# Optimization experiments

Hardware: AMD Instinct MI355X
Metric: run time of the kernel (lower is better)

Reference implementation:

```python
import jax, jax.numpy as jnp
import numpy as np

DIM = 192; HEADS = 6; HDIM = DIM // HEADS
WS = (2, 8, 8); SS = (1, 4, 4)
B, D, H, W = 2, 8, 64, 64
N = WS[0] * WS[1] * WS[2]          # 128 tokens per window
MLP_H = int(DIM * 2.0)
SCALE = HDIM ** -0.5


def _rel_pos_index_np():
    wd, wh, ww = WS
    coords = np.stack(np.meshgrid(np.arange(wd), np.arange(wh), np.arange(ww), indexing='ij'))
    cf = coords.reshape(3, -1)                      # (3, N)
    rel = (cf[:, :, None] - cf[:, None, :]).transpose(1, 2, 0)  # (N, N, 3)
    rel[..., 0] += wd - 1; rel[..., 1] += wh - 1; rel[..., 2] += ww - 1
    rel[..., 0] *= (2 * wh - 1) * (2 * ww - 1)
    rel[..., 1] *= (2 * ww - 1)
    return rel.sum(-1).astype(np.int32)            # (N, N)


def _compute_mask_np():
    wd, wh, ww = WS; sd, sh, sw = SS
    Dp = -(-D // wd) * wd; Hp = -(-H // wh) * wh; Wp = -(-W // ww) * ww
    img = np.zeros((1, Dp, Hp, Wp, 1), np.float32)
    cnt = 0
    for ds in (slice(0, -wd), slice(-wd, -sd), slice(-sd, None)):
        for hs in (slice(0, -wh), slice(-wh, -sh), slice(-sh, None)):
            for vs in (slice(0, -ww), slice(-ww, -sw), slice(-sw, None)):
                img[:, ds, hs, vs, :] = cnt; cnt += 1
    m = img.reshape(1, Dp // wd, wd, Hp // wh, wh, Wp // ww, ww, 1)
    m = m.transpose(0, 1, 3, 5, 2, 4, 6, 7).reshape(-1, N)       # (nW, N)
    am = m[:, None, :] - m[:, :, None]
    return np.where(am != 0, -100.0, 0.0).astype(np.float32)     # (nW, N, N)


def setup_inputs() -> dict:
    key = jax.random.key(0)
    ks = jax.random.split(key, 6)
    f = lambda k, s: (jax.random.normal(k, s, jnp.float32) * 0.02)
    n_bias = (2 * WS[0] - 1) * (2 * WS[1] - 1) * (2 * WS[2] - 1)  # 675
    return dict(
        x=jax.random.normal(ks[0], (B, D, H, W, DIM), jnp.float32),
        mask_matrix=jnp.asarray(_compute_mask_np()),
        rel_pos_index=jnp.asarray(_rel_pos_index_np()),
        gamma1=jnp.ones((DIM,), jnp.float32), beta1=jnp.zeros((DIM,), jnp.float32),
        w_qkv=f(ks[1], (3 * DIM, DIM)), b_qkv=jnp.zeros((3 * DIM,), jnp.float32),
        rpb=f(ks[2], (n_bias, HEADS)),
        w_proj=f(ks[3], (DIM, DIM)), b_proj=jnp.zeros((DIM,), jnp.float32),
        gamma2=jnp.ones((DIM,), jnp.float32), beta2=jnp.zeros((DIM,), jnp.float32),
        w_fc1=f(ks[4], (MLP_H, DIM)), b_fc1=jnp.zeros((MLP_H,), jnp.float32),
        w_fc2=f(ks[5], (DIM, MLP_H)), b_fc2=jnp.zeros((DIM,), jnp.float32),
    )


def _ln(x, g, b, eps=1e-5):
    mu = x.mean(-1, keepdims=True)
    var = ((x - mu) ** 2).mean(-1, keepdims=True)
    return (x - mu) * jax.lax.rsqrt(var + eps) * g + b


def _stl(x, mask, rpi, gamma1, beta1, w_qkv, b_qkv, rpb, w_proj, b_proj,
         gamma2, beta2, w_fc1, b_fc1, w_fc2, b_fc2):
    wd, wh, ww = WS; sd, sh, sw = SS
    # ---- part1: LN -> pad -> roll -> window attention -> reverse ----
    xn = _ln(x, gamma1, beta1)
    pd = (wd - D % wd) % wd; ph = (wh - H % wh) % wh; pw = (ww - W % ww) % ww
    xn = jnp.pad(xn, ((0, 0), (0, pd), (0, ph), (0, pw), (0, 0)))
    Dp, Hp, Wp = D + pd, H + ph, W + pw
    sx = jnp.roll(xn, (-sd, -sh, -sw), axis=(1, 2, 3))
    # window partition -> (Bw, N, C)
    xw = sx.reshape(B, Dp // wd, wd, Hp // wh, wh, Wp // ww, ww, DIM)
    xw = xw.transpose(0, 1, 3, 5, 2, 4, 6, 7).reshape(-1, N, DIM)
    Bw = xw.shape[0]
    qkv = (xw @ w_qkv.T + b_qkv).reshape(Bw, N, 3, HEADS, HDIM).transpose(2, 0, 3, 1, 4)
    q, k, v = qkv[0] * SCALE, qkv[1], qkv[2]
    attn = jnp.einsum('bhnd,bhmd->bhnm', q, k)
    bias = rpb[rpi.reshape(-1)].reshape(N, N, HEADS).transpose(2, 0, 1)  # (H, N, N)
    attn = attn + bias[None]
    nW = mask.shape[0]
    attn = (attn.reshape(Bw // nW, nW, HEADS, N, N) + mask[None, :, None]).reshape(Bw, HEADS, N, N)
    attn = jax.nn.softmax(attn, axis=-1)
    out = jnp.einsum('bhnm,bhmd->bhnd', attn, v).transpose(0, 2, 1, 3).reshape(Bw, N, DIM)
    out = out @ w_proj.T + b_proj
    # window reverse -> un-roll -> slice
    sx = out.reshape(B, Dp // wd, Hp // wh, Wp // ww, wd, wh, ww, DIM)
    sx = sx.transpose(0, 1, 4, 2, 5, 3, 6, 7).reshape(B, Dp, Hp, Wp, DIM)
    part1 = jnp.roll(sx, (sd, sh, sw), axis=(1, 2, 3))[:, :D, :H, :W, :]
    x = x + part1
    # ---- part2: LN -> MLP (GELU, exact) ----
    y = _ln(x, gamma2, beta2)
    h = jax.nn.gelu(y @ w_fc1.T + b_fc1, approximate=False)
    return x + (h @ w_fc2.T + b_fc2)


def reference(x, mask_matrix, rel_pos_index, gamma1, beta1, w_qkv, b_qkv, rpb,
              w_proj, b_proj, gamma2, beta2, w_fc1, b_fc1, w_fc2, b_fc2):
    return _stl(x, mask_matrix, rel_pos_index, gamma1, beta1, w_qkv, b_qkv, rpb,
                w_proj, b_proj, gamma2, beta2, w_fc1, b_fc1, w_fc2, b_fc2)
```

## Files before the change

### kernel.cpp

```cpp
#include <hip/hip_runtime.h>
#include <hip/hip_bf16.h>
#include <math.h>

#define TOKS   65536
#define DIMC   192
#define NTOK   128
#define MLPH   384
#define QSCALE 0.17677669529663687f

typedef unsigned short u16;
typedef unsigned int   u32;
typedef __attribute__((ext_vector_type(8))) short bf16x8;
typedef __attribute__((ext_vector_type(4))) float f32x4;

static __device__ __forceinline__ float gelu_exact(float v) {
    return 0.5f * v * (1.f + erff(v * 0.70710678118654752f));
}
static __device__ __forceinline__ u16 f2bf(float f) {
    __hip_bfloat16 h = __float2bfloat16(f);
    return *reinterpret_cast<u16*>(&h);
}
static __device__ __forceinline__ float bf2f(u16 b) {
    u32 u = ((u32)b) << 16;
    float f;
    __builtin_memcpy(&f, &u, 4);
    return f;
}
static __device__ __forceinline__ void gl_lds16(const u16* g, u16* l) {
    __builtin_amdgcn_global_load_lds(
        (const __attribute__((address_space(1))) void*)g,
        (__attribute__((address_space(3))) void*)l, 16, 0, 0);
}

#define OFF_XW   0u
#define OFF_Q    6291456u
#define OFF_K    12582912u
#define OFF_V    18874368u
#define OFF_BF   25165824u
#define OFF_WB   25264128u

__global__ __launch_bounds__(256) void k_cvt(const float* __restrict__ a,
                                             const float* __restrict__ b,
                                             const float* __restrict__ c,
                                             const float* __restrict__ d,
                                             u16* __restrict__ o) {
    int i = blockIdx.x * 256 + threadIdx.x;
    float v;
    if (i < 110592) v = a[i];
    else if (i < 147456) v = b[i - 110592];
    else if (i < 221184) v = c[i - 147456];
    else v = d[i - 221184];
    o[i] = f2bf(v);
}

__global__ __launch_bounds__(256) void k_bias(const float* __restrict__ rpb,
                                              const int* __restrict__ rpi,
                                              u16* __restrict__ biasw) {
    int idx = blockIdx.x * 256 + threadIdx.x;
    int h = idx >> 14;
    int n = (idx >> 7) & 127;
    int slot = idx & 127;
    int m = ((slot & 7) << 4) + (slot >> 3);
    biasw[idx] = f2bf(rpb[rpi[n * 128 + m] * 6 + h]);
}

template<bool PERMUTE>
__global__ __launch_bounds__(256) void k_ln(const float* __restrict__ x,
                                            const float* __restrict__ gamma,
                                            const float* __restrict__ beta,
                                            u16* __restrict__ out) {
    int tid  = threadIdx.x;
    int lane = tid & 63, wv = tid >> 6;
    int tk = blockIdx.x * 4 + wv;
    size_t src;
    if (PERMUTE) {
        int w_all = tk >> 7, t = tk & 127;
        int b  = w_all >> 8, rem = w_all & 255;
        int di = rem >> 6, hi = (rem >> 3) & 7, wi = rem & 7;
        int qd = (di * 2 + (t >> 6) + 1) & 7;
        int qh = (hi * 8 + ((t >> 3) & 7) + 4) & 63;
        int qw = (wi * 8 + (t & 7) + 4) & 63;
        src = ((size_t)(((b * 8 + qd) * 64 + qh) * 64 + qw)) * DIMC;
    } else {
        src = (size_t)tk * DIMC;
    }
    float v0 = x[src + lane];
    float v1 = x[src + 64 + lane];
    float v2 = x[src + 128 + lane];
    float s  = v0 + v1 + v2;
    float sq = v0 * v0 + v1 * v1 + v2 * v2;
    #pragma unroll
    for (int off = 32; off; off >>= 1) {
        s  += __shfl_xor(s, off);
        sq += __shfl_xor(sq, off);
    }
    float mu   = s * (1.f / 192.f);
    float var  = sq * (1.f / 192.f) - mu * mu;
    float rstd = rsqrtf(var + 1e-5f);
    size_t o = (size_t)tk * DIMC;
    out[o + lane]       = f2bf((v0 - mu) * rstd * gamma[lane]       + beta[lane]);
    out[o + 64 + lane]  = f2bf((v1 - mu) * rstd * gamma[64 + lane]  + beta[64 + lane]);
    out[o + 128 + lane] = f2bf((v2 - mu) * rstd * gamma[128 + lane] + beta[128 + lane]);
}

template<int MODE, int KD>
__global__ __launch_bounds__(256) void k_mgemm(const u16* __restrict__ A,
                                               const u16* __restrict__ W,
                                               const float* __restrict__ bias,
                                               void* __restrict__ outp,
                                               const float* __restrict__ aux,
                                               u16* __restrict__ q_o,
                                               u16* __restrict__ k_o,
                                               u16* __restrict__ v_o) {
    __shared__ u16 As[2][128 * 64];
    const int tid = threadIdx.x;
    const int wv = tid >> 6, l = tid & 63;
    const int l15 = l & 15, g4 = l >> 4;
    const int wm = wv >> 1, wn = wv & 1;
    const size_t m0 = (size_t)blockIdx.x * 128;
    const int n0 = blockIdx.y * 64;
    const int srow = l >> 3, scol = l & 7;

    f32x4 acc[4][2] = {};

    auto STAGE = [&](int b, int t) {
        const u16* Ab = A + m0 * KD + t * 64;
        #pragma unroll
        for (int j = 0; j < 4; ++j) {
            int row = (wv * 4 + j) * 8 + srow;
            int sc  = scol ^ (row & 7);
            gl_lds16(Ab + (size_t)row * KD + sc * 8, &As[b][(wv * 4 + j) * 512]);
        }
    };
    auto COMPUTE = [&](int b, int t) {
        #pragma unroll
        for (int kk = 0; kk < 2; ++kk) {
            bf16x8 bfr[2];
            #pragma unroll
            for (int nt = 0; nt < 2; ++nt)
                bfr[nt] = *(const bf16x8*)&W[(size_t)(n0 + wn * 32 + nt * 16 + l15) * KD
                                             + t * 64 + kk * 32 + g4 * 8];
            #pragma unroll
            for (int mt = 0; mt < 4; ++mt) {
                int row  = wm * 64 + mt * 16 + l15;
                int slot = (kk * 4 + g4) ^ (row & 7);
                bf16x8 afr = *(const bf16x8*)&As[b][row * 64 + slot * 8];
                #pragma unroll
                for (int nt = 0; nt < 2; ++nt)
                    acc[mt][nt] = __builtin_amdgcn_mfma_f32_16x16x32_bf16(afr, bfr[nt],
                                                                          acc[mt][nt], 0, 0, 0);
            }
        }
    };

    constexpr int NT = KD / 64;
    STAGE(0, 0);
    __syncthreads();
    for (int t = 0; t < NT; ++t) {
        if (t + 1 < NT) STAGE((t + 1) & 1, t + 1);
        COMPUTE(t & 1, t);
        __syncthreads();
    }

    #pragma unroll
    for (int mt = 0; mt < 4; ++mt) {
        #pragma unroll
        for (int nt = 0; nt < 2; ++nt) {
            int n  = n0 + wn * 32 + nt * 16 + l15;
            float bb = bias[n];
            int t0 = wm * 64 + mt * 16 + g4 * 4;
            if (MODE == 0) {
                int sel = (n >= 384) ? 2 : (n >= 192 ? 1 : 0);
                int rem = n - sel * 192;
                int head = rem >> 5, dd = rem & 31;
                int w = (int)(m0 >> 7);
                size_t b9 = (size_t)(w * 6 + head) * 4096;
                if (sel < 2) {
                    u16* dst = sel ? k_o : q_o;
                    float scl = sel ? 1.f : QSCALE;
                    #pragma unroll
                    for (int reg = 0; reg < 4; ++reg)
                        dst[b9 + (size_t)(t0 + reg) * 32 + dd] = f2bf((acc[mt][nt][reg] + bb) * scl);
                } else {
                    ushort4 uv;
                    uv.x = f2bf(acc[mt][nt][0] + bb); uv.y = f2bf(acc[mt][nt][1] + bb);
                    uv.z = f2bf(acc[mt][nt][2] + bb); uv.w = f2bf(acc[mt][nt][3] + bb);
                    *(ushort4*)&v_o[b9 + (size_t)dd * 128 + t0] = uv;
                }
            } else if (MODE == 1) {
                float* out = (float*)outp;
                #pragma unroll
                for (int reg = 0; reg < 4; ++reg) {
                    int m = (int)m0 + wm * 64 + mt * 16 + g4 * 4 + reg;
                    int w_all = m >> 7, tt = m & 127;
                    int b  = w_all >> 8, rem = w_all & 255;
                    int di = rem >> 6, hi = (rem >> 3) & 7, wi = rem & 7;
                    int qd = (di * 2 + (tt >> 6) + 1) & 7;
                    int qh = (hi * 8 + ((tt >> 3) & 7) + 4) & 63;
                    int qw = (wi * 8 + (tt & 7) + 4) & 63;
                    size_t dtok = (size_t)(((b * 8 + qd) * 64 + qh) * 64 + qw);
                    out[dtok * DIMC + n] = acc[mt][nt][reg] + bb + aux[dtok * DIMC + n];
                }
            } else if (MODE == 2) {
                u16* out = (u16*)outp;
                #pragma unroll
                for (int reg = 0; reg < 4; ++reg) {
                    size_t m = m0 + t0 + reg;
                    out[m * MLPH + n] = f2bf(gelu_exact(acc[mt][nt][reg] + bb));
                }
            } else {
                float* out = (float*)outp;
                #pragma unroll
                for (int reg = 0; reg < 4; ++reg) {
                    size_t m = m0 + t0 + reg;
                    out[m * DIMC + n] = acc[mt][nt][reg] + bb + aux[m * DIMC + n];
                }
            }
        }
    }
}

__global__ __launch_bounds__(256) void k_attn(const u16* __restrict__ qb,
                                              const u16* __restrict__ kb,
                                              const u16* __restrict__ vb,
                                              const u16* __restrict__ biasw,
                                              u16* __restrict__ attn_out) {
    __shared__ u16 Pl[4][32 * 128];
    int wh = blockIdx.x;
    int w_all = wh / 6, head = wh - w_all * 6;
    int wl = w_all & 255;
    int tid = threadIdx.x;
    int wv = tid >> 6, l = tid & 63;
    int l15 = l & 15, g4 = l >> 4;
    size_t base = (size_t)wh * 4096;
    const u16* qg = qb + base;
    const u16* kg = kb + base;
    const u16* vg = vb + base;
    int rowb = wv * 32;

    bf16x8 qa[2];
    #pragma unroll
    for (int rt = 0; rt < 2; ++rt)
        qa[rt] = *(const bf16x8*)&qg[(size_t)(rowb + rt * 16 + l15) * 32 + g4 * 8];

    f32x4 s[2][8] = {};
    #pragma unroll
    for (int ct = 0; ct < 8; ++ct) {
        bf16x8 kf = *(const bf16x8*)&kg[(size_t)(ct * 16 + l15) * 32 + g4 * 8];
        s[0][ct] = __builtin_amdgcn_mfma_f32_16x16x32_bf16(qa[0], kf, s[0][ct], 0, 0, 0);
        s[1][ct] = __builtin_amdgcn_mfma_f32_16x16x32_bf16(qa[1], kf, s[1][ct], 0, 0, 0);
    }

    int di = wl >> 6, hi = (wl >> 3) & 7, wi = wl & 7;
    auto rcode = [&](int t) {
        int d = di * 2 + (t >> 6);
        int h = hi * 8 + ((t >> 3) & 7);
        int w = wi * 8 + (t & 7);
        int rd = (d < 6) ? 0 : (d < 7 ? 1 : 2);
        int rh = (h < 56) ? 0 : (h < 60 ? 1 : 2);
        int rw = (w < 56) ? 0 : (w < 60 ? 1 : 2);
        return rd * 9 + rh * 3 + rw;
    };
    int rm[8];
    #pragma unroll
    for (int ct = 0; ct < 8; ++ct) rm[ct] = rcode(ct * 16 + l15);

    const u16* bh = biasw + (size_t)head * 16384;
    #pragma unroll
    for (int rt = 0; rt < 2; ++rt)
        #pragma unroll
        for (int reg = 0; reg < 4; ++reg) {
            int n = rowb + rt * 16 + g4 * 4 + reg;
            int rn = rcode(n);
            bf16x8 bv = *(const bf16x8*)&bh[(size_t)n * 128 + l15 * 8];
            #pragma unroll
            for (int ct = 0; ct < 8; ++ct) {
                float mval = (rn == rm[ct]) ? 0.f : -100.f;
                s[rt][ct][reg] += bf2f((u16)bv[ct]) + mval;
            }
        }

    u16* Pw = Pl[wv];
    #pragma unroll
    for (int rt = 0; rt < 2; ++rt)
        #pragma unroll
        for (int reg = 0; reg < 4; ++reg) {
            float mx = -1e30f;
            #pragma unroll
            for (int ct = 0; ct < 8; ++ct) mx = fmaxf(mx, s[rt][ct][reg]);
            #pragma unroll
            for (int off = 1; off < 16; off <<= 1) mx = fmaxf(mx, __shfl_xor(mx, off));
            float sum = 0.f;
            #pragma unroll
            for (int ct = 0; ct < 8; ++ct) {
                float p = __expf(s[rt][ct][reg] - mx);
                s[rt][ct][reg] = p; sum += p;
            }
            #pragma unroll
            for (int off = 1; off < 16; off <<= 1) sum += __shfl_xor(sum, off);
            float inv = 1.f / sum;
            int nloc = rt * 16 + g4 * 4 + reg;
            int sw = ((nloc >> 2) & 3) << 4;
            #pragma unroll
            for (int ct = 0; ct < 8; ++ct) {
                int m = ct * 16 + l15;
                Pw[nloc * 128 + (m ^ sw)] = f2bf(s[rt][ct][reg] * inv);
            }
        }
    __syncthreads();

    f32x4 o[2][2] = {};
    #pragma unroll
    for (int kt = 0; kt < 4; ++kt) {
        bf16x8 vf[2];
        #pragma unroll
        for (int dt = 0; dt < 2; ++dt)
            vf[dt] = *(const bf16x8*)&vg[(size_t)(dt * 16 + l15) * 128 + kt * 32 + g4 * 8];
        #pragma unroll
        for (int rt = 0; rt < 2; ++rt) {
            int nloc = rt * 16 + l15;
            int sw = ((nloc >> 2) & 3) << 4;
            int m8 = kt * 32 + g4 * 8;
            bf16x8 pa = *(const bf16x8*)&Pw[nloc * 128 + (m8 ^ sw)];
            #pragma unroll
            for (int dt = 0; dt < 2; ++dt)
                o[rt][dt] = __builtin_amdgcn_mfma_f32_16x16x32_bf16(pa, vf[dt], o[rt][dt], 0, 0, 0);
        }
    }

    #pragma unroll
    for (int rt = 0; rt < 2; ++rt)
        #pragma unroll
        for (int dt = 0; dt < 2; ++dt)
            #pragma unroll
            for (int reg = 0; reg < 4; ++reg) {
                int n = rowb + rt * 16 + g4 * 4 + reg;
                int d = dt * 16 + l15;
                attn_out[((size_t)(w_all * 128 + n)) * DIMC + head * 32 + d] = f2bf(o[rt][dt][reg]);
            }
}

extern "C" void kernel_launch(void* const* d_in, const int* in_sizes, int n_in,
                              void* d_out, int out_size, void* d_ws, size_t ws_size,
                              hipStream_t stream) {
    const float* x      = (const float*)d_in[0];
    const int*   rpi    = (const int*)d_in[2];
    const float* gamma1 = (const float*)d_in[3];
    const float* beta1  = (const float*)d_in[4];
    const float* w_qkv  = (const float*)d_in[5];
    const float* b_qkv  = (const float*)d_in[6];
    const float* rpb    = (const float*)d_in[7];
    const float* w_proj = (const float*)d_in[8];
    const float* b_proj = (const float*)d_in[9];
    const float* gamma2 = (const float*)d_in[10];
    const float* beta2  = (const float*)d_in[11];
    const float* w_fc1  = (const float*)d_in[12];
    const float* b_fc1  = (const float*)d_in[13];
    const float* w_fc2  = (const float*)d_in[14];
    const float* b_fc2  = (const float*)d_in[15];

    float* ws    = (float*)d_ws;
    u16*   xwu   = (u16*)(ws + OFF_XW);
    u16*   qbu   = (u16*)(ws + OFF_Q);
    u16*   kbu   = (u16*)(ws + OFF_K);
    u16*   vbu   = (u16*)(ws + OFF_V);
    u16*   hbu   = (u16*)(ws + OFF_Q);
    u16*   ybu   = (u16*)(ws + OFF_V);
    u16*   biasw = (u16*)(ws + OFF_BF);
    u16*   wb    = (u16*)(ws + OFF_WB);
    float* xres  = (float*)d_out;

    const u16* wqkv_b = wb;
    const u16* wproj_b = wb + 110592;
    const u16* wfc1_b = wb + 147456;
    const u16* wfc2_b = wb + 221184;

    k_cvt<<<1152, 256, 0, stream>>>(w_qkv, w_proj, w_fc1, w_fc2, wb);
    k_bias<<<384, 256, 0, stream>>>(rpb, rpi, biasw);
    k_ln<true><<<16384, 256, 0, stream>>>(x, gamma1, beta1, xwu);
    k_mgemm<0, 192><<<dim3(512, 9), 256, 0, stream>>>(xwu, wqkv_b, b_qkv, nullptr, nullptr,
                                                      qbu, kbu, vbu);
    k_attn<<<3072, 256, 0, stream>>>(qbu, kbu, vbu, biasw, xwu);
    k_mgemm<1, 192><<<dim3(512, 3), 256, 0, stream>>>(xwu, wproj_b, b_proj, xres, x,
                                                      nullptr, nullptr, nullptr);
    k_ln<false><<<16384, 256, 0, stream>>>(xres, gamma2, beta2, ybu);
    k_mgemm<2, 192><<<dim3(512, 6), 256, 0, stream>>>(ybu, wfc1_b, b_fc1, hbu, nullptr,
                                                      nullptr, nullptr, nullptr);
    k_mgemm<3, 384><<<dim3(512, 3), 256, 0, stream>>>(hbu, wfc2_b, b_fc2, xres, xres,
                                                      nullptr, nullptr, nullptr);
}
```

Baseline: 222.2 us.

## Fuse LayerNorm into GEMM prologues and loop all N tiles per block

The separate LayerNorm kernels are removed. LN1 (with the window permute) and LN2 are now computed directly into the GEMM's shared-memory A tile. Each GEMM block now keeps its full 128x192 (or half of the 384) A panel resident in LDS and loops over every N tile, instead of launching a 2D grid that reloads A for each N tile. This removes two launches and the bf16 round trips of the normalized activations, and cuts repeated A loads. In exchange the grid is only 512 blocks with serial N loops, the old double-buffered staging that overlapped loads with compute is gone, and the LDS footprint grows, which may limit occupancy and latency hiding.

Result: no change. 225.3 us (+1.4%).

```diff
diff --git a/kernel.cpp b/kernel.cpp
--- a/kernel.cpp
+++ b/kernel.cpp
@@ -64,159 +64,172 @@
     biasw[idx] = f2bf(rpb[rpi[n * 128 + m] * 6 + h]);
 }
 
-template<bool PERMUTE>
-__global__ __launch_bounds__(256) void k_ln(const float* __restrict__ x,
-                                            const float* __restrict__ gamma,
-                                            const float* __restrict__ beta,
-                                            u16* __restrict__ out) {
-    int tid  = threadIdx.x;
-    int lane = tid & 63, wv = tid >> 6;
-    int tk = blockIdx.x * 4 + wv;
-    size_t src;
-    if (PERMUTE) {
-        int w_all = tk >> 7, t = tk & 127;
-        int b  = w_all >> 8, rem = w_all & 255;
-        int di = rem >> 6, hi = (rem >> 3) & 7, wi = rem & 7;
-        int qd = (di * 2 + (t >> 6) + 1) & 7;
-        int qh = (hi * 8 + ((t >> 3) & 7) + 4) & 63;
-        int qw = (wi * 8 + (t & 7) + 4) & 63;
-        src = ((size_t)(((b * 8 + qd) * 64 + qh) * 64 + qw)) * DIMC;
-    } else {
-        src = (size_t)tk * DIMC;
-    }
-    float v0 = x[src + lane];
-    float v1 = x[src + 64 + lane];
-    float v2 = x[src + 128 + lane];
-    float s  = v0 + v1 + v2;
-    float sq = v0 * v0 + v1 * v1 + v2 * v2;
-    #pragma unroll
-    for (int off = 32; off; off >>= 1) {
-        s  += __shfl_xor(s, off);
-        sq += __shfl_xor(sq, off);
-    }
-    float mu   = s * (1.f / 192.f);
-    float var  = sq * (1.f / 192.f) - mu * mu;
-    float rstd = rsqrtf(var + 1e-5f);
-    size_t o = (size_t)tk * DIMC;
-    out[o + lane]       = f2bf((v0 - mu) * rstd * gamma[lane]       + beta[lane]);
-    out[o + 64 + lane]  = f2bf((v1 - mu) * rstd * gamma[64 + lane]  + beta[64 + lane]);
-    out[o + 128 + lane] = f2bf((v2 - mu) * rstd * gamma[128 + lane] + beta[128 + lane]);
-}
-
-template<int MODE, int KD>
-__global__ __launch_bounds__(256) void k_mgemm(const u16* __restrict__ A,
-                                               const u16* __restrict__ W,
-                                               const float* __restrict__ bias,
-                                               void* __restrict__ outp,
-                                               const float* __restrict__ aux,
-                                               u16* __restrict__ q_o,
-                                               u16* __restrict__ k_o,
-                                               u16* __restrict__ v_o) {
-    __shared__ u16 As[2][128 * 64];
+template<int MODE>
+__global__ __launch_bounds__(256) void k_fgemm(
+    const void* __restrict__ srcA, const u16* __restrict__ W,
+    const float* __restrict__ bias, void* __restrict__ outp,
+    const float* __restrict__ aux,
+    u16* __restrict__ q_o, u16* __restrict__ k_o, u16* __restrict__ v_o,
+    const float* __restrict__ gam, const float* __restrict__ bet)
+{
+    constexpr int KD = (MODE == 3) ? 384 : 192;
+    constexpr int NT = (MODE == 0) ? 9 : (MODE == 2 ? 6 : 3);
+    __shared__ u16 As[3 * 128 * 64];
     const int tid = threadIdx.x;
     const int wv = tid >> 6, l = tid & 63;
     const int l15 = l & 15, g4 = l >> 4;
     const int wm = wv >> 1, wn = wv & 1;
     const size_t m0 = (size_t)blockIdx.x * 128;
-    const int n0 = blockIdx.y * 64;
-    const int srow = l >> 3, scol = l & 7;
-
-    f32x4 acc[4][2] = {};
-
-    auto STAGE = [&](int b, int t) {
-        const u16* Ab = A + m0 * KD + t * 64;
-        #pragma unroll
-        for (int j = 0; j < 4; ++j) {
-            int row = (wv * 4 + j) * 8 + srow;
-            int sc  = scol ^ (row & 7);
-            gl_lds16(Ab + (size_t)row * KD + sc * 8, &As[b][(wv * 4 + j) * 512]);
+
+    auto STAGEP = [&](int p) {
+        const u16* Ab = (const u16*)srcA + m0 * KD + p * 192;
+        #pragma unroll
+        for (int j = 0; j < 12; ++j) {
+            int cid = j * 256 + wv * 64 + l;
+            int tile = cid >> 10, r = (cid >> 3) & 127, sl = cid & 7;
+            int sc = sl ^ (r & 7);
+            gl_lds16(Ab + (size_t)r * KD + tile * 64 + sc * 8,
+                     &As[(size_t)(j * 256 + wv * 64) * 8]);
         }
     };
-    auto COMPUTE = [&](int b, int t) {
-        #pragma unroll
-        for (int kk = 0; kk < 2; ++kk) {
-            bf16x8 bfr[2];
+
+    if (MODE == 0 || MODE == 2) {
+        const float* xs = (const float*)srcA;
+        float g0 = gam[l], g1 = gam[64 + l], g2 = gam[128 + l];
+        float b0 = bet[l], b1 = bet[64 + l], b2 = bet[128 + l];
+        for (int it = 0; it < 32; ++it) {
+            int t = it * 4 + wv;
+            size_t srcrow;
+            if (MODE == 0) {
+                int w_all = (int)blockIdx.x;
+                int b = w_all >> 8, rem = w_all & 255;
+                int di = rem >> 6, hi = (rem >> 3) & 7, wi = rem & 7;
+                int qd = (di * 2 + (t >> 6) + 1) & 7;
+                int qh = (hi * 8 + ((t >> 3) & 7) + 4) & 63;
+                int qw = (wi * 8 + (t & 7) + 4) & 63;
+                srcrow = ((size_t)(((b * 8 + qd) * 64 + qh) * 64 + qw)) * DIMC;
+            } else {
+                srcrow = (m0 + t) * DIMC;
+            }
+            float v0 = xs[srcrow + l], v1 = xs[srcrow + 64 + l], v2 = xs[srcrow + 128 + l];
+            float s = v0 + v1 + v2, sq = v0 * v0 + v1 * v1 + v2 * v2;
+            #pragma unroll
+            for (int off = 32; off; off >>= 1) { s += __shfl_xor(s, off); sq += __shfl_xor(sq, off); }
+            float mu = s * (1.f / 192.f);
+            float rstd = rsqrtf(sq * (1.f / 192.f) - mu * mu + 1e-5f);
+            int se = (((l >> 3) ^ (t & 7)) << 3) + (l & 7);
+            As[(0 * 128 + t) * 64 + se] = f2bf((v0 - mu) * rstd * g0 + b0);
+            As[(1 * 128 + t) * 64 + se] = f2bf((v1 - mu) * rstd * g1 + b1);
+            As[(2 * 128 + t) * 64 + se] = f2bf((v2 - mu) * rstd * g2 + b2);
+        }
+    } else {
+        STAGEP(0);
+    }
+    __syncthreads();
+
+    auto KSTEP = [&](f32x4 (&acc)[4][2], int n0, int kglob, int ktloc) {
+        bf16x8 bfr[2];
+        #pragma unroll
+        for (int nt = 0; nt < 2; ++nt)
+            bfr[nt] = *(const bf16x8*)&W[(size_t)(n0 + wn * 32 + nt * 16 + l15) * KD
+                                         + kglob * 32 + g4 * 8];
+        #pragma unroll
+        for (int mt = 0; mt < 4; ++mt) {
+            int row  = wm * 64 + mt * 16 + l15;
+            int slot = ((ktloc & 1) * 4 + g4) ^ (row & 7);
+            bf16x8 afr = *(const bf16x8*)&As[(size_t)((ktloc >> 1) * 128 + row) * 64 + slot * 8];
             #pragma unroll
             for (int nt = 0; nt < 2; ++nt)
-                bfr[nt] = *(const bf16x8*)&W[(size_t)(n0 + wn * 32 + nt * 16 + l15) * KD
-                                             + t * 64 + kk * 32 + g4 * 8];
-            #pragma unroll
-            for (int mt = 0; mt < 4; ++mt) {
-                int row  = wm * 64 + mt * 16 + l15;
-                int slot = (kk * 4 + g4) ^ (row & 7);
-                bf16x8 afr = *(const bf16x8*)&As[b][row * 64 + slot * 8];
-                #pragma unroll
-                for (int nt = 0; nt < 2; ++nt)
-                    acc[mt][nt] = __builtin_amdgcn_mfma_f32_16x16x32_bf16(afr, bfr[nt],
-                                                                          acc[mt][nt], 0, 0, 0);
-            }
+                acc[mt][nt] = __builtin_amdgcn_mfma_f32_16x16x32_bf16(afr, bfr[nt],
+                                                                      acc[mt][nt], 0, 0, 0);
         }
     };
 
-    constexpr int NT = KD / 64;
-    STAGE(0, 0);
-    __syncthreads();
-    for (int t = 0; t < NT; ++t) {
-        if (t + 1 < NT) STAGE((t + 1) & 1, t + 1);
-        COMPUTE(t & 1, t);
+    auto EPI = [&](int n0, f32x4 (&acc)[4][2]) {
+        #pragma unroll
+        for (int mt = 0; mt < 4; ++mt) {
+            #pragma unroll
+            for (int nt = 0; nt < 2; ++nt) {
+                int n  = n0 + wn * 32 + nt * 16 + l15;
+                float bb = bias[n];
+                int t0 = wm * 64 + mt * 16 + g4 * 4;
+                if (MODE == 0) {
+                    int sel = (n >= 384) ? 2 : (n >= 192 ? 1 : 0);
+                    int rem = n - sel * 192;
+                    int head = rem >> 5, dd = rem & 31;
+                    int w = (int)blockIdx.x;
+                    size_t b9 = (size_t)(w * 6 + head) * 4096;
+                    if (sel < 2) {
+                        u16* dst = sel ? k_o : q_o;
+                        float scl = sel ? 1.f : QSCALE;
+                        #pragma unroll
+                        for (int reg = 0; reg < 4; ++reg)
+                            dst[b9 + (size_t)(t0 + reg) * 32 + dd] = f2bf((acc[mt][nt][reg] + bb) * scl);
+                    } else {
+                        ushort4 uv;
+                        uv.x = f2bf(acc[mt][nt][0] + bb); uv.y = f2bf(acc[mt][nt][1] + bb);
+                        uv.z = f2bf(acc[mt][nt][2] + bb); uv.w = f2bf(acc[mt][nt][3] + bb);
+                        *(ushort4*)&v_o[b9 + (size_t)dd * 128 + t0] = uv;
+                    }
+                } else if (MODE == 1) {
+                    float* out = (float*)outp;
+                    #pragma unroll
+                    for (int reg = 0; reg < 4; ++reg) {
+                        int m = (int)m0 + t0 + reg;
+                        int w_all = m >> 7, tt = m & 127;
+                        int b  = w_all >> 8, rem = w_all & 255;
+                        int di = rem >> 6, hi = (rem >> 3) & 7, wi = rem & 7;
+                        int qd = (di * 2 + (tt >> 6) + 1) & 7;
+                        int qh = (hi * 8 + ((tt >> 3) & 7) + 4) & 63;
+                        int qw = (wi * 8 + (tt & 7) + 4) & 63;
+                        size_t dtok = (size_t)(((b * 8 + qd) * 64 + qh) * 64 + qw);
+                        out[dtok * DIMC + n] = acc[mt][nt][reg] + bb + aux[dtok * DIMC + n];
+                    }
+                } else if (MODE == 2) {
+                    u16* out = (u16*)outp;
+                    #pragma unroll
+                    for (int reg = 0; reg < 4; ++reg) {
+                        size_t m = m0 + t0 + reg;
+                        out[m * MLPH + n] = f2bf(gelu_exact(acc[mt][nt][reg] + bb));
+                    }
+                } else {
+                    float* out = (float*)outp;
+                    #pragma unroll
+                    for (int reg = 0; reg < 4; ++reg) {
+                        size_t m = m0 + t0 + reg;
+                        out[m * DIMC + n] = acc[mt][nt][reg] + bb + aux[m * DIMC + n];
+                    }
+                }
+            }
+        }
+    };
+
+    if (MODE != 3) {
+        #pragma unroll 1
+        for (int n0i = 0; n0i < NT; ++n0i) {
+            f32x4 acc[4][2] = {};
+            #pragma unroll
+            for (int kt = 0; kt < 6; ++kt) KSTEP(acc, n0i * 64, kt, kt);
+            EPI(n0i * 64, acc);
+        }
+    } else {
+        f32x4 a0[4][2] = {}, a1[4][2] = {}, a2[4][2] = {};
+        #pragma unroll 1
+        for (int kt = 0; kt < 6; ++kt) {
+            KSTEP(a0, 0,   kt, kt);
+            KSTEP(a1, 64,  kt, kt);
+            KSTEP(a2, 128, kt, kt);
+        }
         __syncthreads();
-    }
-
-    #pragma unroll
-    for (int mt = 0; mt < 4; ++mt) {
-        #pragma unroll
-        for (int nt = 0; nt < 2; ++nt) {
-            int n  = n0 + wn * 32 + nt * 16 + l15;
-            float bb = bias[n];
-            int t0 = wm * 64 + mt * 16 + g4 * 4;
-            if (MODE == 0) {
-                int sel = (n >= 384) ? 2 : (n >= 192 ? 1 : 0);
-                int rem = n - sel * 192;
-                int head = rem >> 5, dd = rem & 31;
-                int w = (int)(m0 >> 7);
-                size_t b9 = (size_t)(w * 6 + head) * 4096;
-                if (sel < 2) {
-                    u16* dst = sel ? k_o : q_o;
-                    float scl = sel ? 1.f : QSCALE;
-                    #pragma unroll
-                    for (int reg = 0; reg < 4; ++reg)
-                        dst[b9 + (size_t)(t0 + reg) * 32 + dd] = f2bf((acc[mt][nt][reg] + bb) * scl);
-                } else {
-                    ushort4 uv;
-                    uv.x = f2bf(acc[mt][nt][0] + bb); uv.y = f2bf(acc[mt][nt][1] + bb);
-                    uv.z = f2bf(acc[mt][nt][2] + bb); uv.w = f2bf(acc[mt][nt][3] + bb);
-                    *(ushort4*)&v_o[b9 + (size_t)dd * 128 + t0] = uv;
-                }
-            } else if (MODE == 1) {
-                float* out = (float*)outp;
-                #pragma unroll
-                for (int reg = 0; reg < 4; ++reg) {
-                    int m = (int)m0 + wm * 64 + mt * 16 + g4 * 4 + reg;
-                    int w_all = m >> 7, tt = m & 127;
-                    int b  = w_all >> 8, rem = w_all & 255;
-                    int di = rem >> 6, hi = (rem >> 3) & 7, wi = rem & 7;
-                    int qd = (di * 2 + (tt >> 6) + 1) & 7;
-                    int qh = (hi * 8 + ((tt >> 3) & 7) + 4) & 63;
-                    int qw = (wi * 8 + (tt & 7) + 4) & 63;
-                    size_t dtok = (size_t)(((b * 8 + qd) * 64 + qh) * 64 + qw);
-                    out[dtok * DIMC + n] = acc[mt][nt][reg] + bb + aux[dtok * DIMC + n];
-                }
-            } else if (MODE == 2) {
-                u16* out = (u16*)outp;
-                #pragma unroll
-                for (int reg = 0; reg < 4; ++reg) {
-                    size_t m = m0 + t0 + reg;
-                    out[m * MLPH + n] = f2bf(gelu_exact(acc[mt][nt][reg] + bb));
-                }
-            } else {
-                float* out = (float*)outp;
-                #pragma unroll
-                for (int reg = 0; reg < 4; ++reg) {
-                    size_t m = m0 + t0 + reg;
-                    out[m * DIMC + n] = acc[mt][nt][reg] + bb + aux[m * DIMC + n];
-                }
-            }
-        }
+        STAGEP(1);
+        __syncthreads();
+        #pragma unroll 1
+        for (int kt = 0; kt < 6; ++kt) {
+            KSTEP(a0, 0,   6 + kt, kt);
+            KSTEP(a1, 64,  6 + kt, kt);
+            KSTEP(a2, 128, 6 + kt, kt);
+        }
+        EPI(0, a0); EPI(64, a1); EPI(128, a2);
     }
 }
 
@@ -365,27 +378,24 @@
     u16*   kbu   = (u16*)(ws + OFF_K);
     u16*   vbu   = (u16*)(ws + OFF_V);
     u16*   hbu   = (u16*)(ws + OFF_Q);
-    u16*   ybu   = (u16*)(ws + OFF_V);
     u16*   biasw = (u16*)(ws + OFF_BF);
     u16*   wb    = (u16*)(ws + OFF_WB);
     float* xres  = (float*)d_out;
 
-    const u16* wqkv_b = wb;
+    const u16* wqkv_b  = wb;
     const u16* wproj_b = wb + 110592;
-    const u16* wfc1_b = wb + 147456;
-    const u16* wfc2_b = wb + 221184;
+    const u16* wfc1_b  = wb + 147456;
+    const u16* wfc2_b  = wb + 221184;
 
     k_cvt<<<1152, 256, 0, stream>>>(w_qkv, w_proj, w_fc1, w_fc2, wb);
     k_bias<<<384, 256, 0, stream>>>(rpb, rpi, biasw);
-    k_ln<true><<<16384, 256, 0, stream>>>(x, gamma1, beta1, xwu);
-    k_mgemm<0, 192><<<dim3(512, 9), 256, 0, stream>>>(xwu, wqkv_b, b_qkv, nullptr, nullptr,
-                                                      qbu, kbu, vbu);
+    k_fgemm<0><<<512, 256, 0, stream>>>(x, wqkv_b, b_qkv, nullptr, nullptr,
+                                        qbu, kbu, vbu, gamma1, beta1);
     k_attn<<<3072, 256, 0, stream>>>(qbu, kbu, vbu, biasw, xwu);
-    k_mgemm<1, 192><<<dim3(512, 3), 256, 0, stream>>>(xwu, wproj_b, b_proj, xres, x,
-                                                      nullptr, nullptr, nullptr);
-    k_ln<false><<<16384, 256, 0, stream>>>(xres, gamma2, beta2, ybu);
-    k_mgemm<2, 192><<<dim3(512, 6), 256, 0, stream>>>(ybu, wfc1_b, b_fc1, hbu, nullptr,
-                                                      nullptr, nullptr, nullptr);
-    k_mgemm<3, 384><<<dim3(512, 3), 256, 0, stream>>>(hbu, wfc2_b, b_fc2, xres, xres,
-                                                      nullptr, nullptr, nullptr);
-}
+    k_fgemm<1><<<512, 256, 0, stream>>>(xwu, wproj_b, b_proj, xres, x,
+                                        nullptr, nullptr, nullptr, nullptr, nullptr);
+    k_fgemm<2><<<512, 256, 0, stream>>>(xres, wfc1_b, b_fc1, hbu, nullptr,
+                                        nullptr, nullptr, nullptr, gamma2, beta2);
+    k_fgemm<3><<<512, 256, 0, stream>>>(hbu, wfc2_b, b_fc2, xres, xres,
+                                        nullptr, nullptr, nullptr, nullptr, nullptr);
+}
```

## Restructure GEMMs to keep weight tile in LDS and stream A into registers

Applied to the files above, without the earlier changes.

Replaces the A-in-LDS double-buffered GEMM with a kernel that loads the block's full 64-column weight slice into LDS once. Each block then processes several 128-row M tiles, reading A fragments straight from global memory into registers, with the next tile's loads issued while the current tile computes. This amortizes weight staging across 2-4 M tiles and removes the per-K-step barrier. The cost is fewer blocks, which lowers parallelism, plus heavy register use for the A fragments, which may lower occupancy.

Result: slower. 237.2 us (+6.8%).

```diff
diff --git a/kernel.cpp b/kernel.cpp
--- a/kernel.cpp
+++ b/kernel.cpp
@@ -30,6 +30,10 @@
     __builtin_amdgcn_global_load_lds(
         (const __attribute__((address_space(1))) void*)g,
         (__attribute__((address_space(3))) void*)l, 16, 0, 0);
+}
+static __device__ __forceinline__ f32x4 fz4() {
+    f32x4 z = {0.f, 0.f, 0.f, 0.f};
+    return z;
 }
 
 #define OFF_XW   0u
@@ -103,120 +107,159 @@
     out[o + 128 + lane] = f2bf((v2 - mu) * rstd * gamma[128 + lane] + beta[128 + lane]);
 }
 
-template<int MODE, int KD>
-__global__ __launch_bounds__(256) void k_mgemm(const u16* __restrict__ A,
-                                               const u16* __restrict__ W,
-                                               const float* __restrict__ bias,
-                                               void* __restrict__ outp,
-                                               const float* __restrict__ aux,
-                                               u16* __restrict__ q_o,
-                                               u16* __restrict__ k_o,
-                                               u16* __restrict__ v_o) {
-    __shared__ u16 As[2][128 * 64];
+template<int MODE>
+__global__ __launch_bounds__(256) void k_wgemm(
+    const u16* __restrict__ A, const u16* __restrict__ W,
+    const float* __restrict__ bias, void* __restrict__ outp,
+    const float* __restrict__ aux,
+    u16* __restrict__ q_o, u16* __restrict__ k_o, u16* __restrict__ v_o)
+{
+    constexpr int KD = (MODE == 3) ? 384 : 192;
+    constexpr int KT = KD / 64;
+    constexpr int NS = (MODE == 1 || MODE == 3) ? 2 : 4;
+    __shared__ u16 Ws[KT * 64 * 64];
     const int tid = threadIdx.x;
     const int wv = tid >> 6, l = tid & 63;
     const int l15 = l & 15, g4 = l >> 4;
-    const int wm = wv >> 1, wn = wv & 1;
-    const size_t m0 = (size_t)blockIdx.x * 128;
     const int n0 = blockIdx.y * 64;
-    const int srow = l >> 3, scol = l & 7;
-
-    f32x4 acc[4][2] = {};
-
-    auto STAGE = [&](int b, int t) {
-        const u16* Ab = A + m0 * KD + t * 64;
-        #pragma unroll
-        for (int j = 0; j < 4; ++j) {
-            int row = (wv * 4 + j) * 8 + srow;
-            int sc  = scol ^ (row & 7);
-            gl_lds16(Ab + (size_t)row * KD + sc * 8, &As[b][(wv * 4 + j) * 512]);
-        }
+
+    {
+        const u16* Wb = W + (size_t)n0 * KD;
+        #pragma unroll
+        for (int j = 0; j < KT * 2; ++j) {
+            int cid = j * 256 + tid;
+            int tile = cid >> 9, r = (cid >> 3) & 63, sl = cid & 7;
+            int sc = sl ^ (r & 7);
+            gl_lds16(Wb + (size_t)r * KD + tile * 64 + sc * 8,
+                     &Ws[(size_t)(j * 256 + wv * 64) * 8]);
+        }
+    }
+
+    f32x4 acc[2][4];
+    #pragma unroll
+    for (int mt = 0; mt < 2; ++mt)
+        #pragma unroll
+        for (int nt = 0; nt < 4; ++nt) acc[mt][nt] = fz4();
+
+    bf16x8 afA[2][6], afB[2][6];
+
+    auto LOADA = [&](bf16x8 (&af)[2][6], size_t m0, int kh) {
+        const u16* Ab = A + (m0 + (size_t)(wv * 32 + l15)) * KD + kh * 192;
+        #pragma unroll
+        for (int mt = 0; mt < 2; ++mt)
+            #pragma unroll
+            for (int kg = 0; kg < 6; ++kg)
+                af[mt][kg] = *(const bf16x8*)&Ab[(size_t)mt * 16 * KD + kg * 32 + g4 * 8];
     };
-    auto COMPUTE = [&](int b, int t) {
-        #pragma unroll
-        for (int kk = 0; kk < 2; ++kk) {
-            bf16x8 bfr[2];
-            #pragma unroll
-            for (int nt = 0; nt < 2; ++nt)
-                bfr[nt] = *(const bf16x8*)&W[(size_t)(n0 + wn * 32 + nt * 16 + l15) * KD
-                                             + t * 64 + kk * 32 + g4 * 8];
-            #pragma unroll
-            for (int mt = 0; mt < 4; ++mt) {
-                int row  = wm * 64 + mt * 16 + l15;
-                int slot = (kk * 4 + g4) ^ (row & 7);
-                bf16x8 afr = *(const bf16x8*)&As[b][row * 64 + slot * 8];
-                #pragma unroll
-                for (int nt = 0; nt < 2; ++nt)
-                    acc[mt][nt] = __builtin_amdgcn_mfma_f32_16x16x32_bf16(afr, bfr[nt],
-                                                                          acc[mt][nt], 0, 0, 0);
+    auto COMP = [&](bf16x8 (&af)[2][6], int kbase) {
+        #pragma unroll
+        for (int kg = 0; kg < 6; ++kg) {
+            int kgg = kbase + kg;
+            #pragma unroll
+            for (int nt = 0; nt < 4; ++nt) {
+                int r = nt * 16 + l15;
+                int slot = ((kgg & 1) * 4 + g4) ^ (r & 7);
+                bf16x8 wf = *(const bf16x8*)&Ws[(kgg >> 1) * 4096 + r * 64 + slot * 8];
+                acc[0][nt] = __builtin_amdgcn_mfma_f32_16x16x32_bf16(af[0][kg], wf, acc[0][nt], 0, 0, 0);
+                acc[1][nt] = __builtin_amdgcn_mfma_f32_16x16x32_bf16(af[1][kg], wf, acc[1][nt], 0, 0, 0);
             }
         }
     };
-
-    constexpr int NT = KD / 64;
-    STAGE(0, 0);
-    __syncthreads();
-    for (int t = 0; t < NT; ++t) {
-        if (t + 1 < NT) STAGE((t + 1) & 1, t + 1);
-        COMPUTE(t & 1, t);
+    auto ZERO = [&]() {
+        #pragma unroll
+        for (int mt = 0; mt < 2; ++mt)
+            #pragma unroll
+            for (int nt = 0; nt < 4; ++nt) acc[mt][nt] = fz4();
+    };
+    auto EPI = [&](size_t m0) {
+        int w = (int)(m0 >> 7);
+        #pragma unroll
+        for (int mt = 0; mt < 2; ++mt) {
+            int t0 = wv * 32 + mt * 16 + g4 * 4;
+            #pragma unroll
+            for (int nt = 0; nt < 4; ++nt) {
+                int n = n0 + nt * 16 + l15;
+                float bb = bias[n];
+                if (MODE == 0) {
+                    int sel = (n0 >= 384) ? 2 : (n0 >= 192 ? 1 : 0);
+                    int rem = n - sel * 192;
+                    int head = rem >> 5, dd = rem & 31;
+                    size_t b9 = (size_t)(w * 6 + head) * 4096;
+                    if (sel < 2) {
+                        u16* dst = sel ? k_o : q_o;
+                        float scl = sel ? 1.f : QSCALE;
+                        #pragma unroll
+                        for (int reg = 0; reg < 4; ++reg)
+                            dst[b9 + (size_t)(t0 + reg) * 32 + dd] =
+                                f2bf((acc[mt][nt][reg] + bb) * scl);
+                    } else {
+                        ushort4 uv;
+                        uv.x = f2bf(acc[mt][nt][0] + bb); uv.y = f2bf(acc[mt][nt][1] + bb);
+                        uv.z = f2bf(acc[mt][nt][2] + bb); uv.w = f2bf(acc[mt][nt][3] + bb);
+                        *(ushort4*)&v_o[b9 + (size_t)dd * 128 + t0] = uv;
+                    }
+                } else if (MODE == 1) {
+                    float* out = (float*)outp;
+                    #pragma unroll
+                    for (int reg = 0; reg < 4; ++reg) {
+                        int m = (int)m0 + t0 + reg;
+                        int w_all = m >> 7, tt = m & 127;
+                        int b  = w_all >> 8, rem = w_all & 255;
+                        int di = rem >> 6, hi = (rem >> 3) & 7, wi = rem & 7;
+                        int qd = (di * 2 + (tt >> 6) + 1) & 7;
+                        int qh = (hi * 8 + ((tt >> 3) & 7) + 4) & 63;
+                        int qw = (wi * 8 + (tt & 7) + 4) & 63;
+                        size_t dtok = (size_t)(((b * 8 + qd) * 64 + qh) * 64 + qw);
+                        out[dtok * DIMC + n] = acc[mt][nt][reg] + bb + aux[dtok * DIMC + n];
+                    }
+                } else if (MODE == 2) {
+                    u16* out = (u16*)outp;
+                    #pragma unroll
+                    for (int reg = 0; reg < 4; ++reg) {
+                        size_t m = m0 + t0 + reg;
+                        out[m * MLPH + n] = f2bf(gelu_exact(acc[mt][nt][reg] + bb));
+                    }
+                } else {
+                    float* out = (float*)outp;
+                    #pragma unroll
+                    for (int reg = 0; reg < 4; ++reg) {
+                        size_t m = m0 + t0 + reg;
+                        out[m * DIMC + n] = acc[mt][nt][reg] + bb + aux[m * DIMC + n];
+                    }
+                }
+            }
+        }
+    };
+
+    const size_t s0 = (size_t)blockIdx.x * NS * 128;
+    if (MODE == 3) {
+        LOADA(afA, s0, 0);
+        LOADA(afB, s0, 1);
         __syncthreads();
-    }
-
-    #pragma unroll
-    for (int mt = 0; mt < 4; ++mt) {
-        #pragma unroll
-        for (int nt = 0; nt < 2; ++nt) {
-            int n  = n0 + wn * 32 + nt * 16 + l15;
-            float bb = bias[n];
-            int t0 = wm * 64 + mt * 16 + g4 * 4;
-            if (MODE == 0) {
-                int sel = (n >= 384) ? 2 : (n >= 192 ? 1 : 0);
-                int rem = n - sel * 192;
-                int head = rem >> 5, dd = rem & 31;
-                int w = (int)(m0 >> 7);
-                size_t b9 = (size_t)(w * 6 + head) * 4096;
-                if (sel < 2) {
-                    u16* dst = sel ? k_o : q_o;
-                    float scl = sel ? 1.f : QSCALE;
-                    #pragma unroll
-                    for (int reg = 0; reg < 4; ++reg)
-                        dst[b9 + (size_t)(t0 + reg) * 32 + dd] = f2bf((acc[mt][nt][reg] + bb) * scl);
-                } else {
-                    ushort4 uv;
-                    uv.x = f2bf(acc[mt][nt][0] + bb); uv.y = f2bf(acc[mt][nt][1] + bb);
-                    uv.z = f2bf(acc[mt][nt][2] + bb); uv.w = f2bf(acc[mt][nt][3] + bb);
-                    *(ushort4*)&v_o[b9 + (size_t)dd * 128 + t0] = uv;
-                }
-            } else if (MODE == 1) {
-                float* out = (float*)outp;
-                #pragma unroll
-                for (int reg = 0; reg < 4; ++reg) {
-                    int m = (int)m0 + wm * 64 + mt * 16 + g4 * 4 + reg;
-                    int w_all = m >> 7, tt = m & 127;
-                    int b  = w_all >> 8, rem = w_all & 255;
-                    int di = rem >> 6, hi = (rem >> 3) & 7, wi = rem & 7;
-                    int qd = (di * 2 + (tt >> 6) + 1) & 7;
-                    int qh = (hi * 8 + ((tt >> 3) & 7) + 4) & 63;
-                    int qw = (wi * 8 + (tt & 7) + 4) & 63;
-                    size_t dtok = (size_t)(((b * 8 + qd) * 64 + qh) * 64 + qw);
-                    out[dtok * DIMC + n] = acc[mt][nt][reg] + bb + aux[dtok * DIMC + n];
-                }
-            } else if (MODE == 2) {
-                u16* out = (u16*)outp;
-                #pragma unroll
-                for (int reg = 0; reg < 4; ++reg) {
-                    size_t m = m0 + t0 + reg;
-                    out[m * MLPH + n] = f2bf(gelu_exact(acc[mt][nt][reg] + bb));
-                }
-            } else {
-                float* out = (float*)outp;
-                #pragma unroll
-                for (int reg = 0; reg < 4; ++reg) {
-                    size_t m = m0 + t0 + reg;
-                    out[m * DIMC + n] = acc[mt][nt][reg] + bb + aux[m * DIMC + n];
-                }
-            }
-        }
+        COMP(afA, 0);
+        LOADA(afA, s0 + 128, 0);
+        COMP(afB, 6);
+        EPI(s0); ZERO();
+        LOADA(afB, s0 + 128, 1);
+        COMP(afA, 0);
+        COMP(afB, 6);
+        EPI(s0 + 128);
+    } else if (MODE == 1) {
+        LOADA(afA, s0, 0);
+        LOADA(afB, s0 + 128, 0);
+        __syncthreads();
+        COMP(afA, 0); EPI(s0); ZERO();
+        COMP(afB, 0); EPI(s0 + 128);
+    } else {
+        LOADA(afA, s0, 0);
+        LOADA(afB, s0 + 128, 0);
+        __syncthreads();
+        COMP(afA, 0); EPI(s0); ZERO();
+        LOADA(afA, s0 + 256, 0);
+        COMP(afB, 0); EPI(s0 + 128); ZERO();
+        LOADA(afB, s0 + 384, 0);
+        COMP(afA, 0); EPI(s0 + 256); ZERO();
+        COMP(afB, 0); EPI(s0 + 384);
     }
 }
 
@@ -370,22 +413,22 @@
     u16*   wb    = (u16*)(ws + OFF_WB);
     float* xres  = (float*)d_out;
 
-    const u16* wqkv_b = wb;
+    const u16* wqkv_b  = wb;
     const u16* wproj_b = wb + 110592;
-    const u16* wfc1_b = wb + 147456;
-    const u16* wfc2_b = wb + 221184;
+    const u16* wfc1_b  = wb + 147456;
+    const u16* wfc2_b  = wb + 221184;
 
     k_cvt<<<1152, 256, 0, stream>>>(w_qkv, w_proj, w_fc1, w_fc2, wb);
     k_bias<<<384, 256, 0, stream>>>(rpb, rpi, biasw);
     k_ln<true><<<16384, 256, 0, stream>>>(x, gamma1, beta1, xwu);
-    k_mgemm<0, 192><<<dim3(512, 9), 256, 0, stream>>>(xwu, wqkv_b, b_qkv, nullptr, nullptr,
-                                                      qbu, kbu, vbu);
+    k_wgemm<0><<<dim3(128, 9), 256, 0, stream>>>(xwu, wqkv_b, b_qkv, nullptr, nullptr,
+                                                 qbu, kbu, vbu);
     k_attn<<<3072, 256, 0, stream>>>(qbu, kbu, vbu, biasw, xwu);
-    k_mgemm<1, 192><<<dim3(512, 3), 256, 0, stream>>>(xwu, wproj_b, b_proj, xres, x,
-                                                      nullptr, nullptr, nullptr);
+    k_wgemm<1><<<dim3(256, 3), 256, 0, stream>>>(xwu, wproj_b, b_proj, xres, x,
+                                                 nullptr, nullptr, nullptr);
     k_ln<false><<<16384, 256, 0, stream>>>(xres, gamma2, beta2, ybu);
-    k_mgemm<2, 192><<<dim3(512, 6), 256, 0, stream>>>(ybu, wfc1_b, b_fc1, hbu, nullptr,
-                                                      nullptr, nullptr, nullptr);
-    k_mgemm<3, 384><<<dim3(512, 3), 256, 0, stream>>>(hbu, wfc2_b, b_fc2, xres, xres,
-                                                      nullptr, nullptr, nullptr);
-}
+    k_wgemm<2><<<dim3(128, 6), 256, 0, stream>>>(ybu, wfc1_b, b_fc1, hbu, nullptr,
+                                                 nullptr, nullptr, nullptr);
+    k_wgemm<3><<<dim3(256, 3), 256, 0, stream>>>(hbu, wfc2_b, b_fc2, xres, xres,
+                                                 nullptr, nullptr, nullptr);
+}
```

## Stage GEMM and attention epilogues through LDS for vectorized coalesced stores

Applied to the files above, without the earlier changes.

The GEMM epilogues now write their accumulators into the freed shared-memory tile with an XOR swizzle, then read back whole rows and issue 16-byte vectorized global stores. This covers the q/k/v scatter, the GELU output, and the fp32 residual adds, which also load aux as float4. The attention kernel's output likewise goes through LDS so each thread stores 8 bf16 at once instead of scattered 2-byte writes. The goal is to remove uncoalesced narrow global writes, at the cost of extra barriers and LDS round trips in the epilogue.

Measured after the change: 216.7 us. 1.03x faster.

```diff
diff --git a/kernel.cpp b/kernel.cpp
--- a/kernel.cpp
+++ b/kernel.cpp
@@ -113,6 +113,8 @@
                                                u16* __restrict__ k_o,
                                                u16* __restrict__ v_o) {
     __shared__ u16 As[2][128 * 64];
+    u16*   Eu = (u16*)As;
+    float* Ef = (float*)As;
     const int tid = threadIdx.x;
     const int wv = tid >> 6, l = tid & 63;
     const int l15 = l & 15, g4 = l >> 4;
@@ -162,60 +164,109 @@
         __syncthreads();
     }
 
-    #pragma unroll
-    for (int mt = 0; mt < 4; ++mt) {
-        #pragma unroll
-        for (int nt = 0; nt < 2; ++nt) {
-            int n  = n0 + wn * 32 + nt * 16 + l15;
-            float bb = bias[n];
-            int t0 = wm * 64 + mt * 16 + g4 * 4;
-            if (MODE == 0) {
-                int sel = (n >= 384) ? 2 : (n >= 192 ? 1 : 0);
-                int rem = n - sel * 192;
-                int head = rem >> 5, dd = rem & 31;
-                int w = (int)(m0 >> 7);
-                size_t b9 = (size_t)(w * 6 + head) * 4096;
-                if (sel < 2) {
-                    u16* dst = sel ? k_o : q_o;
-                    float scl = sel ? 1.f : QSCALE;
-                    #pragma unroll
-                    for (int reg = 0; reg < 4; ++reg)
-                        dst[b9 + (size_t)(t0 + reg) * 32 + dd] = f2bf((acc[mt][nt][reg] + bb) * scl);
-                } else {
-                    ushort4 uv;
-                    uv.x = f2bf(acc[mt][nt][0] + bb); uv.y = f2bf(acc[mt][nt][1] + bb);
-                    uv.z = f2bf(acc[mt][nt][2] + bb); uv.w = f2bf(acc[mt][nt][3] + bb);
-                    *(ushort4*)&v_o[b9 + (size_t)dd * 128 + t0] = uv;
-                }
-            } else if (MODE == 1) {
-                float* out = (float*)outp;
+    const int w = (int)(m0 >> 7);
+
+    if (MODE == 0 || MODE == 2) {
+        const int sel = (MODE == 0) ? ((n0 >= 384) ? 2 : (n0 >= 192 ? 1 : 0)) : 0;
+        const float scl = (MODE == 0 && sel == 0) ? QSCALE : 1.f;
+        #pragma unroll
+        for (int mt = 0; mt < 4; ++mt) {
+            #pragma unroll
+            for (int nt = 0; nt < 2; ++nt) {
+                int c = wn * 32 + nt * 16 + l15;
+                float bb = bias[n0 + c];
                 #pragma unroll
                 for (int reg = 0; reg < 4; ++reg) {
-                    int m = (int)m0 + wm * 64 + mt * 16 + g4 * 4 + reg;
-                    int w_all = m >> 7, tt = m & 127;
-                    int b  = w_all >> 8, rem = w_all & 255;
-                    int di = rem >> 6, hi = (rem >> 3) & 7, wi = rem & 7;
-                    int qd = (di * 2 + (tt >> 6) + 1) & 7;
-                    int qh = (hi * 8 + ((tt >> 3) & 7) + 4) & 63;
-                    int qw = (wi * 8 + (tt & 7) + 4) & 63;
-                    size_t dtok = (size_t)(((b * 8 + qd) * 64 + qh) * 64 + qw);
-                    out[dtok * DIMC + n] = acc[mt][nt][reg] + bb + aux[dtok * DIMC + n];
+                    int r = wm * 64 + mt * 16 + g4 * 4 + reg;
+                    float v = acc[mt][nt][reg] + bb;
+                    if (MODE == 2) v = gelu_exact(v);
+                    else v *= scl;
+                    int slot8 = (c >> 3) ^ ((r >> 2) & 7);
+                    Eu[r * 64 + slot8 * 8 + (c & 7)] = f2bf(v);
                 }
-            } else if (MODE == 2) {
-                u16* out = (u16*)outp;
+            }
+        }
+        __syncthreads();
+        if (MODE == 2) {
+            u16* out = (u16*)outp;
+            #pragma unroll
+            for (int p = 0; p < 4; ++p) {
+                int cid = p * 256 + tid;
+                int r = cid >> 3, j = cid & 7;
+                int slot8 = j ^ ((r >> 2) & 7);
+                bf16x8 vv = *(const bf16x8*)&Eu[r * 64 + slot8 * 8];
+                *(bf16x8*)&out[(m0 + r) * MLPH + n0 + j * 8] = vv;
+            }
+        } else if (sel < 2) {
+            u16* dst = sel ? k_o : q_o;
+            const int hbase = (n0 - sel * 192) >> 5;
+            #pragma unroll
+            for (int p = 0; p < 4; ++p) {
+                int cid = p * 256 + tid;
+                int r = cid >> 3, j = cid & 7;
+                int c0 = j * 8;
+                int slot8 = j ^ ((r >> 2) & 7);
+                bf16x8 vv = *(const bf16x8*)&Eu[r * 64 + slot8 * 8];
+                size_t b9 = (size_t)(w * 6 + hbase + (c0 >> 5)) * 4096;
+                *(bf16x8*)&dst[b9 + (size_t)r * 32 + (c0 & 31)] = vv;
+            }
+        } else {
+            const int hbase = (n0 - 384) >> 5;
+            #pragma unroll
+            for (int p = 0; p < 4; ++p) {
+                int cid = p * 256 + tid;
+                int c = cid >> 4, jt = cid & 15;
+                int t0 = jt * 8;
+                u16 tmp[8];
+                #pragma unroll
+                for (int i = 0; i < 8; ++i) {
+                    int r = t0 + i;
+                    int slot8 = (c >> 3) ^ ((r >> 2) & 7);
+                    tmp[i] = Eu[r * 64 + slot8 * 8 + (c & 7)];
+                }
+                size_t b9 = (size_t)(w * 6 + hbase + (c >> 5)) * 4096;
+                *(bf16x8*)&v_o[b9 + (size_t)(c & 31) * 128 + t0] = *(bf16x8*)tmp;
+            }
+        }
+    } else {
+        #pragma unroll
+        for (int mt = 0; mt < 4; ++mt) {
+            #pragma unroll
+            for (int nt = 0; nt < 2; ++nt) {
+                int c = wn * 32 + nt * 16 + l15;
+                float bb = bias[n0 + c];
                 #pragma unroll
                 for (int reg = 0; reg < 4; ++reg) {
-                    size_t m = m0 + t0 + reg;
-                    out[m * MLPH + n] = f2bf(gelu_exact(acc[mt][nt][reg] + bb));
+                    int r = wm * 64 + mt * 16 + g4 * 4 + reg;
+                    int swz = (c >> 2) ^ ((r >> 2) & 3);
+                    Ef[r * 64 + swz * 4 + (c & 3)] = acc[mt][nt][reg] + bb;
                 }
+            }
+        }
+        __syncthreads();
+        float* out = (float*)outp;
+        #pragma unroll
+        for (int p = 0; p < 8; ++p) {
+            int cid = p * 256 + tid;
+            int r = cid >> 4, j = cid & 15;
+            int swz = j ^ ((r >> 2) & 3);
+            float4 vv = *(const float4*)&Ef[r * 64 + swz * 4];
+            size_t drow;
+            if (MODE == 1) {
+                int m = (int)m0 + r;
+                int w_all = m >> 7, tt = m & 127;
+                int b  = w_all >> 8, rem = w_all & 255;
+                int di = rem >> 6, hi = (rem >> 3) & 7, wi = rem & 7;
+                int qd = (di * 2 + (tt >> 6) + 1) & 7;
+                int qh = (hi * 8 + ((tt >> 3) & 7) + 4) & 63;
+                int qw = (wi * 8 + (tt & 7) + 4) & 63;
+                drow = (size_t)(((b * 8 + qd) * 64 + qh) * 64 + qw) * DIMC;
             } else {
-                float* out = (float*)outp;
-                #pragma unroll
-                for (int reg = 0; reg < 4; ++reg) {
-                    size_t m = m0 + t0 + reg;
-                    out[m * DIMC + n] = acc[mt][nt][reg] + bb + aux[m * DIMC + n];
-                }
-            }
+                drow = (m0 + r) * DIMC;
+            }
+            float4 ax = *(const float4*)&aux[drow + n0 + j * 4];
+            vv.x += ax.x; vv.y += ax.y; vv.z += ax.z; vv.w += ax.w;
+            *(float4*)&out[drow + n0 + j * 4] = vv;
         }
     }
 }
@@ -226,6 +277,7 @@
                                               const u16* __restrict__ biasw,
                                               u16* __restrict__ attn_out) {
     __shared__ u16 Pl[4][32 * 128];
+    u16* Ou = (u16*)Pl;
     int wh = blockIdx.x;
     int w_all = wh / 6, head = wh - w_all * 6;
     int wl = w_all & 255;
@@ -328,16 +380,27 @@
         }
     }
 
+    __syncthreads();
     #pragma unroll
     for (int rt = 0; rt < 2; ++rt)
         #pragma unroll
         for (int dt = 0; dt < 2; ++dt)
             #pragma unroll
             for (int reg = 0; reg < 4; ++reg) {
-                int n = rowb + rt * 16 + g4 * 4 + reg;
-                int d = dt * 16 + l15;
-                attn_out[((size_t)(w_all * 128 + n)) * DIMC + head * 32 + d] = f2bf(o[rt][dt][reg]);
-            }
+                int r = rowb + rt * 16 + g4 * 4 + reg;
+                int c = dt * 16 + l15;
+                int slot8 = (c >> 3) ^ ((r >> 2) & 3);
+                Ou[r * 32 + slot8 * 8 + (c & 7)] = f2bf(o[rt][dt][reg]);
+            }
+    __syncthreads();
+    #pragma unroll
+    for (int p = 0; p < 2; ++p) {
+        int cid = p * 256 + tid;
+        int r = cid >> 2, j = cid & 3;
+        int slot8 = j ^ ((r >> 2) & 3);
+        bf16x8 vv = *(const bf16x8*)&Ou[r * 32 + slot8 * 8];
+        *(bf16x8*)&attn_out[((size_t)(w_all * 128 + r)) * DIMC + head * 32 + j * 8] = vv;
+    }
 }
 
 extern "C" void kernel_launch(void* const* d_in, const int* in_sizes, int n_in,
@@ -370,10 +433,10 @@
     u16*   wb    = (u16*)(ws + OFF_WB);
     float* xres  = (float*)d_out;
 
-    const u16* wqkv_b = wb;
+    const u16* wqkv_b  = wb;
     const u16* wproj_b = wb + 110592;
-    const u16* wfc1_b = wb + 147456;
-    const u16* wfc2_b = wb + 221184;
+    const u16* wfc1_b  = wb + 147456;
+    const u16* wfc2_b  = wb + 221184;
 
     k_cvt<<<1152, 256, 0, stream>>>(w_qkv, w_proj, w_fc1, w_fc2, wb);
     k_bias<<<384, 256, 0, stream>>>(rpb, rpi, biasw);
```
